# Performance work log

Measured on AMD Instinct MI355X. Metric: run time of the kernel, lower is better.

## Reference

```python
import jax, jax.numpy as jnp
import numpy as np


def setup_inputs() -> dict:
    key = jax.random.key(0)
    k1, k2, k3, k4, k5 = jax.random.split(key, 5)
    B, H, W, C = 4, 64, 64, 512
    x = jax.random.normal(k1, (B, H, W, C), dtype=jnp.float32)
    # 1x1 conv kernels (no bias), he_normal-ish scaling
    W1 = jax.random.normal(k2, (C, C // 8), dtype=jnp.float32) * (2.0 / C) ** 0.5
    W2 = jax.random.normal(k3, (C, C // 8), dtype=jnp.float32) * (2.0 / C) ** 0.5
    W3 = jax.random.normal(k4, (C, C), dtype=jnp.float32) * (2.0 / C) ** 0.5
    gamma = jax.random.normal(k5, (1,), dtype=jnp.float32) * 0.1
    return {"x": x, "W1": W1, "W2": W2, "W3": W3, "gamma": gamma}


def reference(x, W1, W2, W3, gamma):
    B, H, W, C = x.shape
    HW = H * W
    Cr = C // 8
    # 1x1 convs == per-position channel projections
    b = jnp.einsum('bhwc,cd->bhwd', x, W1).reshape(B, HW, Cr)   # queries
    c = jnp.einsum('bhwc,cd->bhwd', x, W2).reshape(B, HW, Cr)   # keys
    d = jnp.einsum('bhwc,cd->bhwd', x, W3).reshape(B, HW, C)    # values
    # bc[b,i,j] = <b_i, c_j>  (no 1/sqrt(d) scaling, per original)
    bc = jnp.einsum('bik,bjk->bij', b, c)                        # [B, HW, HW]
    sm = jax.nn.softmax(bc, axis=-1)
    # keras dot(axes=[1,2]): contract HW axis of d with last axis of sm -> [B, C, HW]
    bcd = jnp.einsum('bjc,bij->bci', d, sm)                      # [B, C, HW]
    # original applies a raw Reshape (NOT a transpose) to (h, w, C) — faithful
    bcd = bcd.reshape(B, H, W, C)
    return gamma * bcd + x
```

## Files before the change

### kernel.cpp

```cpp
#include <hip/hip_runtime.h>
#include <hip/hip_bf16.h>
#include <stdint.h>

typedef __bf16 bf16x8 __attribute__((ext_vector_type(8)));
typedef unsigned short ushort8 __attribute__((ext_vector_type(8)));
typedef unsigned short ushort4v __attribute__((ext_vector_type(4)));
typedef float f32x4 __attribute__((ext_vector_type(4)));

#define MFMA16(a, b, c) __builtin_amdgcn_mfma_f32_16x16x32_bf16((a), (b), (c), 0, 0, 0)

__device__ __forceinline__ unsigned short f2bf(float f) {
    uint32_t u = __float_as_uint(f);
    u += 0x7FFFu + ((u >> 16) & 1u);
    return (unsigned short)(u >> 16);
}
__device__ __forceinline__ float bf2f(unsigned short u) {
    return __uint_as_float(((uint32_t)u) << 16);
}

__global__ void k_build_wt(const float* __restrict__ W1, const float* __restrict__ W2,
                           const float* __restrict__ W3, unsigned short* __restrict__ Wt) {
    int idx = blockIdx.x * 256 + threadIdx.x;
    int n = idx >> 9;
    int k = idx & 511;
    float v;
    if (n < 64)       v = W1[k * 64 + n];
    else if (n < 128) v = W2[k * 64 + (n - 64)];
    else              v = W3[k * 512 + (n - 128)];
    Wt[idx] = f2bf(v);
}

__global__ __launch_bounds__(512, 2) void k_proj(const float* __restrict__ x,
                                                 const unsigned short* __restrict__ Wt,
                                                 unsigned short* __restrict__ Qb,
                                                 unsigned short* __restrict__ Kb,
                                                 unsigned short* __restrict__ Vt) {
    __shared__ __align__(16) unsigned short As[64 * 520];
    const int tid  = threadIdx.x;
    const int lane = tid & 63;
    const int w    = tid >> 6;
    const int m0   = blockIdx.x * 64;
    const int col  = lane & 15, quad = lane >> 4;

#pragma unroll
    for (int itr = 0; itr < 16; ++itr) {
        int idx = itr * 512 + tid;
        int row = idx >> 7, c4 = (idx & 127) << 2;
        f32x4 v = *(const f32x4*)(x + (m0 + row) * 512 + c4);
        ushort4v o;
        o[0] = f2bf(v[0]); o[1] = f2bf(v[1]); o[2] = f2bf(v[2]); o[3] = f2bf(v[3]);
        *(ushort4v*)(&As[row * 520 + c4]) = o;
    }
    __syncthreads();

    f32x4 acc[4][5] = {};
    bf16x8 bcur[5], bnxt[5];
    const unsigned short* bp = Wt + quad * 8;
#pragma unroll
    for (int nt = 0; nt < 5; ++nt)
        bcur[nt] = *(const bf16x8*)(bp + (w * 80 + nt * 16 + col) * 512);

    for (int k = 0; k < 16; ++k) {
        int kn = (k + 1) & 15;
#pragma unroll
        for (int nt = 0; nt < 5; ++nt)
            bnxt[nt] = *(const bf16x8*)(bp + (w * 80 + nt * 16 + col) * 512 + kn * 32);
        bf16x8 af[4];
#pragma unroll
        for (int it = 0; it < 4; ++it)
            af[it] = *(const bf16x8*)(&As[(it * 16 + col) * 520 + k * 32 + quad * 8]);
#pragma unroll
        for (int it = 0; it < 4; ++it)
#pragma unroll
            for (int nt = 0; nt < 5; ++nt)
                acc[it][nt] = MFMA16(af[it], bcur[nt], acc[it][nt]);
#pragma unroll
        for (int nt = 0; nt < 5; ++nt) bcur[nt] = bnxt[nt];
    }

#pragma unroll
    for (int nt = 0; nt < 5; ++nt) {
        int n0 = w * 80 + nt * 16;
        if (n0 < 128) {
            unsigned short* dst = (n0 < 64) ? Qb : Kb;
            int nc = (n0 < 64) ? (n0 + col) : (n0 - 64 + col);
#pragma unroll
            for (int it = 0; it < 4; ++it) {
                int ig = m0 + it * 16 + quad * 4;
#pragma unroll
                for (int r = 0; r < 4; ++r)
                    dst[(ig + r) * 64 + nc] = f2bf(acc[it][nt][r]);
            }
        } else {
            int vrow = n0 - 128 + col;
#pragma unroll
            for (int it = 0; it < 4; ++it) {
                int ig = m0 + it * 16 + quad * 4;
                int b = ig >> 12, ii = ig & 4095;
                ushort4v pk;
#pragma unroll
                for (int r = 0; r < 4; ++r) pk[r] = f2bf(acc[it][nt][r]);
                *(ushort4v*)(Vt + ((b * 512 + vrow) << 12) + ii) = pk;
            }
        }
    }
}

__global__ __launch_bounds__(512, 2) void k_flash(const unsigned short* __restrict__ Qb,
                                                  const unsigned short* __restrict__ Kb,
                                                  const unsigned short* __restrict__ Vt,
                                                  unsigned short* __restrict__ Op,
                                                  float* __restrict__ ml) {
    __shared__ __align__(16) unsigned short Qs[128 * 72];
    __shared__ __align__(16) float          Ss[128 * 132];
    __shared__ __align__(16) unsigned short Ps[128 * 136];
    __shared__ float m_s[128], l_s[128], al_s[128];

    const int tid  = threadIdx.x;
    const int lane = tid & 63;
    const int w    = tid >> 6;
    const int col  = lane & 15, quad = lane >> 4;
    const int xcd  = blockIdx.x & 7;
    const int b    = xcd >> 1;
    const int jh   = xcd & 1;
    const int i0   = (blockIdx.x >> 3) * 128;

    const unsigned short* Qbase = Qb + (b * 4096 + i0) * 64;
    const unsigned short* Kbase = Kb + b * 4096 * 64;
    const unsigned short* Vbase = Vt + b * 512 * 4096;

    if (tid < 128) { m_s[tid] = -3.0e38f; l_s[tid] = 0.0f; }
    {
#pragma unroll
        for (int half = 0; half < 2; ++half) {
            int row = half * 64 + (tid >> 3), ch = tid & 7;
            *(ushort8*)(&Qs[row * 72 + ch * 8]) =
                *(const ushort8*)(Qbase + row * 64 + ch * 8);
        }
    }
    __syncthreads();

    f32x4 acc[8][4] = {};

    for (int jj = 0; jj < 16; ++jj) {
        const int j0 = jh * 2048 + jj * 128;
        {
            const unsigned short* kp = Kbase + (j0 + w * 16 + col) * 64 + quad * 8;
            bf16x8 kf0 = *(const bf16x8*)(kp);
            bf16x8 kf1 = *(const bf16x8*)(kp + 32);
#pragma unroll
            for (int it = 0; it < 8; ++it) {
                bf16x8 q0 = *(const bf16x8*)(&Qs[(it * 16 + col) * 72 + quad * 8]);
                bf16x8 q1 = *(const bf16x8*)(&Qs[(it * 16 + col) * 72 + 32 + quad * 8]);
                f32x4 s = {};
                s = MFMA16(q0, kf0, s);
                s = MFMA16(q1, kf1, s);
                int rb = it * 16 + quad * 4;
#pragma unroll
                for (int r = 0; r < 4; ++r) Ss[(rb + r) * 132 + w * 16 + col] = s[r];
            }
        }
        bf16x8 vf0[4][2];
#pragma unroll
        for (int ct = 0; ct < 4; ++ct) {
            const unsigned short* vp = Vbase + (w * 64 + ct * 16 + col) * 4096 + j0 + quad * 8;
            vf0[ct][0] = *(const bf16x8*)(vp);
            vf0[ct][1] = *(const bf16x8*)(vp + 32);
        }
        __syncthreads();
        {
            int row = tid >> 2, g = tid & 3;
            float* spA = &Ss[row * 132 + g * 16];
            float* spB = &Ss[row * 132 + (g + 4) * 16];
            f32x4 v0 = *(f32x4*)(spA + 0);
            f32x4 v1 = *(f32x4*)(spA + 4);
            f32x4 v2 = *(f32x4*)(spA + 8);
            f32x4 v3 = *(f32x4*)(spA + 12);
            f32x4 u0 = *(f32x4*)(spB + 0);
            f32x4 u1 = *(f32x4*)(spB + 4);
            f32x4 u2 = *(f32x4*)(spB + 8);
            f32x4 u3 = *(f32x4*)(spB + 12);
            float mx = fmaxf(fmaxf(fmaxf(v0[0], v0[1]), fmaxf(v0[2], v0[3])),
                             fmaxf(fmaxf(v1[0], v1[1]), fmaxf(v1[2], v1[3])));
            mx = fmaxf(mx, fmaxf(fmaxf(fmaxf(v2[0], v2[1]), fmaxf(v2[2], v2[3])),
                                 fmaxf(fmaxf(v3[0], v3[1]), fmaxf(v3[2], v3[3]))));
            mx = fmaxf(mx, fmaxf(fmaxf(fmaxf(u0[0], u0[1]), fmaxf(u0[2], u0[3])),
                                 fmaxf(fmaxf(u1[0], u1[1]), fmaxf(u1[2], u1[3]))));
            mx = fmaxf(mx, fmaxf(fmaxf(fmaxf(u2[0], u2[1]), fmaxf(u2[2], u2[3])),
                                 fmaxf(fmaxf(u3[0], u3[1]), fmaxf(u3[2], u3[3]))));
            mx = fmaxf(mx, __shfl_xor(mx, 1, 4));
            mx = fmaxf(mx, __shfl_xor(mx, 2, 4));
            float mo = m_s[row];
            float mn = fmaxf(mo, mx);
            float al = __expf(mo - mn);
#pragma unroll
            for (int i = 0; i < 4; ++i) {
                v0[i] = __expf(v0[i] - mn); v1[i] = __expf(v1[i] - mn);
                v2[i] = __expf(v2[i] - mn); v3[i] = __expf(v3[i] - mn);
                u0[i] = __expf(u0[i] - mn); u1[i] = __expf(u1[i] - mn);
                u2[i] = __expf(u2[i] - mn); u3[i] = __expf(u3[i] - mn);
            }
            float sum = (v0[0]+v0[1]+v0[2]+v0[3]) + (v1[0]+v1[1]+v1[2]+v1[3])
                      + (v2[0]+v2[1]+v2[2]+v2[3]) + (v3[0]+v3[1]+v3[2]+v3[3])
                      + (u0[0]+u0[1]+u0[2]+u0[3]) + (u1[0]+u1[1]+u1[2]+u1[3])
                      + (u2[0]+u2[1]+u2[2]+u2[3]) + (u3[0]+u3[1]+u3[2]+u3[3]);
            ushort8 p0, p1, p2, p3;
#pragma unroll
            for (int i = 0; i < 4; ++i) {
                p0[i] = f2bf(v0[i]); p0[i + 4] = f2bf(v1[i]);
                p1[i] = f2bf(v2[i]); p1[i + 4] = f2bf(v3[i]);
                p2[i] = f2bf(u0[i]); p2[i + 4] = f2bf(u1[i]);
                p3[i] = f2bf(u2[i]); p3[i + 4] = f2bf(u3[i]);
            }
            *(ushort8*)(&Ps[row * 136 + g * 16])           = p0;
            *(ushort8*)(&Ps[row * 136 + g * 16 + 8])       = p1;
            *(ushort8*)(&Ps[row * 136 + (g + 4) * 16])     = p2;
            *(ushort8*)(&Ps[row * 136 + (g + 4) * 16 + 8]) = p3;
            sum += __shfl_xor(sum, 1, 4);
            sum += __shfl_xor(sum, 2, 4);
            if (g == 0) { m_s[row] = mn; l_s[row] = al * l_s[row] + sum; al_s[row] = al; }
        }
        __syncthreads();
#pragma unroll
        for (int it = 0; it < 8; ++it) {
            int rb = it * 16 + quad * 4;
            f32x4 av;
            av[0] = al_s[rb]; av[1] = al_s[rb + 1]; av[2] = al_s[rb + 2]; av[3] = al_s[rb + 3];
#pragma unroll
            for (int ct = 0; ct < 4; ++ct) acc[it][ct] *= av;
        }
        __builtin_amdgcn_s_setprio(1);
#pragma unroll
        for (int it = 0; it < 8; ++it) {
            bf16x8 pf0 = *(const bf16x8*)(&Ps[(it * 16 + col) * 136 + quad * 8]);
            bf16x8 pf1 = *(const bf16x8*)(&Ps[(it * 16 + col) * 136 + 32 + quad * 8]);
#pragma unroll
            for (int ct = 0; ct < 4; ++ct) {
                acc[it][ct] = MFMA16(pf0, vf0[ct][0], acc[it][ct]);
                acc[it][ct] = MFMA16(pf1, vf0[ct][1], acc[it][ct]);
            }
        }
        __builtin_amdgcn_s_setprio(0);
        bf16x8 vf1[4][2];
#pragma unroll
        for (int ct = 0; ct < 4; ++ct) {
            const unsigned short* vp = Vbase + (w * 64 + ct * 16 + col) * 4096 + j0 + quad * 8;
            vf1[ct][0] = *(const bf16x8*)(vp + 64);
            vf1[ct][1] = *(const bf16x8*)(vp + 96);
        }
        __builtin_amdgcn_s_setprio(1);
#pragma unroll
        for (int it = 0; it < 8; ++it) {
            bf16x8 pf2 = *(const bf16x8*)(&Ps[(it * 16 + col) * 136 + 64 + quad * 8]);
            bf16x8 pf3 = *(const bf16x8*)(&Ps[(it * 16 + col) * 136 + 96 + quad * 8]);
#pragma unroll
            for (int ct = 0; ct < 4; ++ct) {
                acc[it][ct] = MFMA16(pf2, vf1[ct][0], acc[it][ct]);
                acc[it][ct] = MFMA16(pf3, vf1[ct][1], acc[it][ct]);
            }
        }
        __builtin_amdgcn_s_setprio(0);
    }

    unsigned short* obh = Op + jh * 8388608 + b * 2097152;
#pragma unroll
    for (int it = 0; it < 8; ++it) {
        int rb = it * 16 + quad * 4;
#pragma unroll
        for (int ct = 0; ct < 4; ++ct) {
            int cg = w * 64 + ct * 16 + col;
            int f = cg * 4096 + i0 + rb;
            ushort4v pk;
            f32x4 a = acc[it][ct];
#pragma unroll
            for (int r = 0; r < 4; ++r) pk[r] = f2bf(a[r]);
            *(ushort4v*)(obh + f) = pk;
        }
    }
    if (tid < 128) {
        float2 v; v.x = m_s[tid]; v.y = l_s[tid];
        ((float2*)ml)[(jh * 4 + b) * 4096 + i0 + tid] = v;
    }
}

__global__ void k_mlw(const float* __restrict__ ml, const float* __restrict__ gamma,
                      float* __restrict__ cw) {
    int t = blockIdx.x * 256 + threadIdx.x;
    float2 a = ((const float2*)ml)[t];
    float2 c = ((const float2*)ml)[16384 + t];
    float M = fmaxf(a.x, c.x);
    float e0 = __expf(a.x - M), e1 = __expf(c.x - M);
    float g = gamma[0] / (e0 * a.y + e1 * c.y);
    float2 o; o.x = g * e0; o.y = g * e1;
    ((float2*)cw)[t] = o;
}

__global__ void k_combine(const unsigned short* __restrict__ Op,
                          const float* __restrict__ cw,
                          const float* __restrict__ x, float* __restrict__ out) {
    int t = blockIdx.x * 256 + threadIdx.x;
    int f = t << 2;
    int b = f >> 21, i = f & 4095;
    const float* cwf = cw + (((b << 12) + i) << 1);
    f32x4 wa = *(const f32x4*)(cwf);
    f32x4 wb = *(const f32x4*)(cwf + 4);
    ushort4v o0 = *(const ushort4v*)(Op + f);
    ushort4v o1 = *(const ushort4v*)(Op + 8388608 + f);
    f32x4 xv = *(const f32x4*)(x + f);
    f32x4 o;
    o[0] = wa[0] * bf2f(o0[0]) + wa[1] * bf2f(o1[0]) + xv[0];
    o[1] = wa[2] * bf2f(o0[1]) + wa[3] * bf2f(o1[1]) + xv[1];
    o[2] = wb[0] * bf2f(o0[2]) + wb[1] * bf2f(o1[2]) + xv[2];
    o[3] = wb[2] * bf2f(o0[3]) + wb[3] * bf2f(o1[3]) + xv[3];
    *(f32x4*)(out + f) = o;
}

extern "C" void kernel_launch(void* const* d_in, const int* in_sizes, int n_in,
                              void* d_out, int out_size, void* d_ws, size_t ws_size,
                              hipStream_t stream) {
    const float* x  = (const float*)d_in[0];
    const float* W1 = (const float*)d_in[1];
    const float* W2 = (const float*)d_in[2];
    const float* W3 = (const float*)d_in[3];
    const float* gm = (const float*)d_in[4];
    float* out = (float*)d_out;

    char* ws = (char*)d_ws;
    unsigned short* Wt = (unsigned short*)(ws);
    unsigned short* Qb = (unsigned short*)(ws + (1u  << 20));
    unsigned short* Kb = (unsigned short*)(ws + (3u  << 20));
    unsigned short* Vt = (unsigned short*)(ws + (5u  << 20));
    unsigned short* Op = (unsigned short*)(ws + (21u << 20));
    float*          ml = (float*)        (ws + (53u << 20));
    float*          cw = (float*)        (ws + (53u << 20) + 262144);

    hipLaunchKernelGGL(k_build_wt, dim3(1280), dim3(256), 0, stream, W1, W2, W3, Wt);
    hipLaunchKernelGGL(k_proj,     dim3(256),  dim3(512), 0, stream, x, Wt, Qb, Kb, Vt);
    hipLaunchKernelGGL(k_flash,    dim3(256),  dim3(512), 0, stream, Qb, Kb, Vt, Op, ml);
    hipLaunchKernelGGL(k_mlw,      dim3(64),   dim3(256), 0, stream, ml, gm, cw);
    hipLaunchKernelGGL(k_combine,  dim3(8192), dim3(256), 0, stream, Op, cw, x, out);
}
```

Measured before the change: 225.9 us.

## Halve flash query tile to 64 rows with 4 waves and double the block count

The flash kernel now uses 64 query rows per block with 256 threads (4 waves) instead of 128 rows with 512 threads, and launches 512 blocks instead of 256. Each wave covers 128 output channels and 32 key columns, and the PV loop is restructured into four k-steps that prefetch the next V fragments into registers while the current MFMAs run. The intent is better occupancy and CU balance from more, smaller blocks, plus latency hiding on the V loads. The trade-off is that each block re-reads K and V for half as many query rows, doubling global K/V traffic, and the larger per-wave accumulator and V register arrays raise register pressure.

After: 268.2 us. +18.7%, slower.

```diff
diff --git a/kernel.cpp b/kernel.cpp
--- a/kernel.cpp
+++ b/kernel.cpp
@@ -106,15 +106,15 @@
     }
 }
 
-__global__ __launch_bounds__(512, 2) void k_flash(const unsigned short* __restrict__ Qb,
+__global__ __launch_bounds__(256, 2) void k_flash(const unsigned short* __restrict__ Qb,
                                                   const unsigned short* __restrict__ Kb,
                                                   const unsigned short* __restrict__ Vt,
                                                   unsigned short* __restrict__ Op,
                                                   float* __restrict__ ml) {
-    __shared__ __align__(16) unsigned short Qs[128 * 72];
-    __shared__ __align__(16) float          Ss[128 * 132];
-    __shared__ __align__(16) unsigned short Ps[128 * 136];
-    __shared__ float m_s[128], l_s[128], al_s[128];
+    __shared__ __align__(16) unsigned short Qs[64 * 72];
+    __shared__ __align__(16) float          Ss[64 * 132];
+    __shared__ __align__(16) unsigned short Ps[64 * 136];
+    __shared__ float m_s[64], l_s[64], al_s[64];
 
     const int tid  = threadIdx.x;
     const int lane = tid & 63;
@@ -123,50 +123,56 @@
     const int xcd  = blockIdx.x & 7;
     const int b    = xcd >> 1;
     const int jh   = xcd & 1;
-    const int i0   = (blockIdx.x >> 3) * 128;
+    const int i0   = (blockIdx.x >> 3) * 64;
 
     const unsigned short* Qbase = Qb + (b * 4096 + i0) * 64;
     const unsigned short* Kbase = Kb + b * 4096 * 64;
     const unsigned short* Vbase = Vt + b * 512 * 4096;
 
-    if (tid < 128) { m_s[tid] = -3.0e38f; l_s[tid] = 0.0f; }
+    if (tid < 64) { m_s[tid] = -3.0e38f; l_s[tid] = 0.0f; }
     {
 #pragma unroll
-        for (int half = 0; half < 2; ++half) {
-            int row = half * 64 + (tid >> 3), ch = tid & 7;
+        for (int p = 0; p < 2; ++p) {
+            int row = p * 32 + (tid >> 3), ch = tid & 7;
             *(ushort8*)(&Qs[row * 72 + ch * 8]) =
                 *(const ushort8*)(Qbase + row * 64 + ch * 8);
         }
     }
     __syncthreads();
 
-    f32x4 acc[8][4] = {};
+    f32x4 acc[4][8] = {};
 
     for (int jj = 0; jj < 16; ++jj) {
         const int j0 = jh * 2048 + jj * 128;
         {
-            const unsigned short* kp = Kbase + (j0 + w * 16 + col) * 64 + quad * 8;
-            bf16x8 kf0 = *(const bf16x8*)(kp);
-            bf16x8 kf1 = *(const bf16x8*)(kp + 32);
-#pragma unroll
-            for (int it = 0; it < 8; ++it) {
+            bf16x8 kf[2][2];
+#pragma unroll
+            for (int nc = 0; nc < 2; ++nc) {
+                const unsigned short* kp = Kbase + (j0 + w * 32 + nc * 16 + col) * 64 + quad * 8;
+                kf[nc][0] = *(const bf16x8*)(kp);
+                kf[nc][1] = *(const bf16x8*)(kp + 32);
+            }
+#pragma unroll
+            for (int it = 0; it < 4; ++it) {
                 bf16x8 q0 = *(const bf16x8*)(&Qs[(it * 16 + col) * 72 + quad * 8]);
                 bf16x8 q1 = *(const bf16x8*)(&Qs[(it * 16 + col) * 72 + 32 + quad * 8]);
-                f32x4 s = {};
-                s = MFMA16(q0, kf0, s);
-                s = MFMA16(q1, kf1, s);
                 int rb = it * 16 + quad * 4;
 #pragma unroll
-                for (int r = 0; r < 4; ++r) Ss[(rb + r) * 132 + w * 16 + col] = s[r];
-            }
-        }
-        bf16x8 vf0[4][2];
-#pragma unroll
-        for (int ct = 0; ct < 4; ++ct) {
-            const unsigned short* vp = Vbase + (w * 64 + ct * 16 + col) * 4096 + j0 + quad * 8;
-            vf0[ct][0] = *(const bf16x8*)(vp);
-            vf0[ct][1] = *(const bf16x8*)(vp + 32);
-        }
+                for (int nc = 0; nc < 2; ++nc) {
+                    f32x4 s = {};
+                    s = MFMA16(q0, kf[nc][0], s);
+                    s = MFMA16(q1, kf[nc][1], s);
+#pragma unroll
+                    for (int r = 0; r < 4; ++r)
+                        Ss[(rb + r) * 132 + w * 32 + nc * 16 + col] = s[r];
+                }
+            }
+        }
+        const unsigned short* vpb = Vbase + (w * 128 + col) * 4096 + j0 + quad * 8;
+        bf16x8 vfA[8];
+#pragma unroll
+        for (int ct = 0; ct < 8; ++ct)
+            vfA[ct] = *(const bf16x8*)(vpb + ct * 16 * 4096);
         __syncthreads();
         {
             int row = tid >> 2, g = tid & 3;
@@ -222,53 +228,44 @@
         }
         __syncthreads();
 #pragma unroll
-        for (int it = 0; it < 8; ++it) {
+        for (int it = 0; it < 4; ++it) {
             int rb = it * 16 + quad * 4;
             f32x4 av;
             av[0] = al_s[rb]; av[1] = al_s[rb + 1]; av[2] = al_s[rb + 2]; av[3] = al_s[rb + 3];
 #pragma unroll
-            for (int ct = 0; ct < 4; ++ct) acc[it][ct] *= av;
-        }
-        __builtin_amdgcn_s_setprio(1);
-#pragma unroll
-        for (int it = 0; it < 8; ++it) {
-            bf16x8 pf0 = *(const bf16x8*)(&Ps[(it * 16 + col) * 136 + quad * 8]);
-            bf16x8 pf1 = *(const bf16x8*)(&Ps[(it * 16 + col) * 136 + 32 + quad * 8]);
-#pragma unroll
-            for (int ct = 0; ct < 4; ++ct) {
-                acc[it][ct] = MFMA16(pf0, vf0[ct][0], acc[it][ct]);
-                acc[it][ct] = MFMA16(pf1, vf0[ct][1], acc[it][ct]);
-            }
-        }
-        __builtin_amdgcn_s_setprio(0);
-        bf16x8 vf1[4][2];
-#pragma unroll
-        for (int ct = 0; ct < 4; ++ct) {
-            const unsigned short* vp = Vbase + (w * 64 + ct * 16 + col) * 4096 + j0 + quad * 8;
-            vf1[ct][0] = *(const bf16x8*)(vp + 64);
-            vf1[ct][1] = *(const bf16x8*)(vp + 96);
-        }
-        __builtin_amdgcn_s_setprio(1);
-#pragma unroll
-        for (int it = 0; it < 8; ++it) {
-            bf16x8 pf2 = *(const bf16x8*)(&Ps[(it * 16 + col) * 136 + 64 + quad * 8]);
-            bf16x8 pf3 = *(const bf16x8*)(&Ps[(it * 16 + col) * 136 + 96 + quad * 8]);
-#pragma unroll
-            for (int ct = 0; ct < 4; ++ct) {
-                acc[it][ct] = MFMA16(pf2, vf1[ct][0], acc[it][ct]);
-                acc[it][ct] = MFMA16(pf3, vf1[ct][1], acc[it][ct]);
-            }
-        }
-        __builtin_amdgcn_s_setprio(0);
+            for (int ct = 0; ct < 8; ++ct) acc[it][ct] *= av;
+        }
+#pragma unroll
+        for (int kk = 0; kk < 4; ++kk) {
+            bf16x8 vfB[8];
+            if (kk < 3) {
+#pragma unroll
+                for (int ct = 0; ct < 8; ++ct)
+                    vfB[ct] = *(const bf16x8*)(vpb + ct * 16 * 4096 + (kk + 1) * 32);
+            }
+            __builtin_amdgcn_s_setprio(1);
+#pragma unroll
+            for (int it = 0; it < 4; ++it) {
+                bf16x8 pf = *(const bf16x8*)(&Ps[(it * 16 + col) * 136 + kk * 32 + quad * 8]);
+#pragma unroll
+                for (int ct = 0; ct < 8; ++ct)
+                    acc[it][ct] = MFMA16(pf, vfA[ct], acc[it][ct]);
+            }
+            __builtin_amdgcn_s_setprio(0);
+            if (kk < 3) {
+#pragma unroll
+                for (int ct = 0; ct < 8; ++ct) vfA[ct] = vfB[ct];
+            }
+        }
     }
 
     unsigned short* obh = Op + jh * 8388608 + b * 2097152;
 #pragma unroll
-    for (int it = 0; it < 8; ++it) {
+    for (int it = 0; it < 4; ++it) {
         int rb = it * 16 + quad * 4;
 #pragma unroll
-        for (int ct = 0; ct < 4; ++ct) {
-            int cg = w * 64 + ct * 16 + col;
+        for (int ct = 0; ct < 8; ++ct) {
+            int cg = w * 128 + ct * 16 + col;
             int f = cg * 4096 + i0 + rb;
             ushort4v pk;
             f32x4 a = acc[it][ct];
@@ -277,7 +274,7 @@
             *(ushort4v*)(obh + f) = pk;
         }
     }
-    if (tid < 128) {
+    if (tid < 64) {
         float2 v; v.x = m_s[tid]; v.y = l_s[tid];
         ((float2*)ml)[(jh * 4 + b) * 4096 + i0 + tid] = v;
     }
@@ -336,7 +333,7 @@
 
     hipLaunchKernelGGL(k_build_wt, dim3(1280), dim3(256), 0, stream, W1, W2, W3, Wt);
     hipLaunchKernelGGL(k_proj,     dim3(256),  dim3(512), 0, stream, x, Wt, Qb, Kb, Vt);
-    hipLaunchKernelGGL(k_flash,    dim3(256),  dim3(512), 0, stream, Qb, Kb, Vt, Op, ml);
+    hipLaunchKernelGGL(k_flash,    dim3(512),  dim3(256), 0, stream, Qb, Kb, Vt, Op, ml);
     hipLaunchKernelGGL(k_mlw,      dim3(64),   dim3(256), 0, stream, ml, gm, cw);
     hipLaunchKernelGGL(k_combine,  dim3(8192), dim3(256), 0, stream, Op, cw, x, out);
 }
```
